# Optimization experiments

Hardware: AMD Instinct MI355X
Metric: run time of the kernel (lower is better)

## Reference

```python
import jax, jax.numpy as jnp
import numpy as np

EPS = 1e-3  # Q = eps * I(5) in the original module

def setup_inputs() -> dict:
    key = jax.random.key(0)
    k1, k2, k3 = jax.random.split(key, 3)
    B, n = 4194304, 5
    x = jax.random.normal(k1, (B, n), dtype=jnp.float32)
    # fc1 = nn.Linear(n, n): weight [n, n], bias [n]
    W = jax.random.normal(k2, (n, n), dtype=jnp.float32) * (1.0 / np.sqrt(n))
    b_fc = jax.random.normal(k3, (n,), dtype=jnp.float32) * 0.1
    return {"x": x, "W": W, "b_fc": b_fc}

def reference(x, W, b_fc):
    # h = fc1(x)  (the QP inequality RHS per sample)
    h = x @ W.T + b_fc  # [B, 5]
    # Per-sample QP: min_z 0.5*eps*||z||^2 + 1^T z  s.t.  -z <= h  (G = -I)
    # Separable closed form (exact solution cvxopt converges to):
    #   unconstrained minimizer z_i = -1/eps; constraint z_i >= -h_i
    #   => z_i = max(-h_i, -1/eps)
    z = jnp.maximum(-h, -1.0 / EPS)  # [B, 5] primal solutions
    return z
```

## Files before the change

kernel.cpp:

```cpp
#include <hip/hip_runtime.h>


#define BLOCK 256
#define WAVES_PER_BLOCK 4
#define F4_PER_WAVE 320

typedef float vf4 __attribute__((ext_vector_type(4)));

__global__ __launch_bounds__(BLOCK) void qpnet_kernel(
    const float* __restrict__ x,
    const float* __restrict__ W,
    const float* __restrict__ bfc,
    float* __restrict__ out,
    int total_f4)
{
    __shared__ __align__(16) float lds[BLOCK * 20];

    float w[5][5];
    float bias[5];
#pragma unroll
    for (int j = 0; j < 5; ++j) {
        bias[j] = bfc[j];
#pragma unroll
        for (int i = 0; i < 5; ++i) w[j][i] = W[j * 5 + i];
    }

    const int wave = threadIdx.x >> 6;
    const int lane = threadIdx.x & 63;
    float* __restrict__ wlds = &lds[wave * (64 * 20)];

    const int wave_id = blockIdx.x * WAVES_PER_BLOCK + wave;
    const int wbase = wave_id * F4_PER_WAVE;
    if (wbase >= total_f4) return;

    const vf4* __restrict__ xin  = reinterpret_cast<const vf4*>(x);
    vf4* __restrict__       zout = reinterpret_cast<vf4*>(out);

#pragma unroll
    for (int k = 0; k < 5; ++k) {
        *reinterpret_cast<vf4*>(&wlds[(k * 64 + lane) * 4]) = xin[wbase + k * 64 + lane];
    }
    asm volatile("s_waitcnt lgkmcnt(0)" ::: "memory");

    float v[20];
#pragma unroll
    for (int p = 0; p < 5; ++p) {
        *reinterpret_cast<vf4*>(&v[4 * p]) =
            *reinterpret_cast<const vf4*>(&wlds[lane * 20 + 4 * p]);
    }

#pragma unroll
    for (int k = 0; k < 4; ++k) {
        float t0 = bias[0], t1 = bias[1], t2 = bias[2], t3 = bias[3], t4 = bias[4];
#pragma unroll
        for (int i = 0; i < 5; ++i) {
            const float xv = v[k * 5 + i];
            t0 = fmaf(xv, w[0][i], t0);
            t1 = fmaf(xv, w[1][i], t1);
            t2 = fmaf(xv, w[2][i], t2);
            t3 = fmaf(xv, w[3][i], t3);
            t4 = fmaf(xv, w[4][i], t4);
        }
        v[k * 5 + 0] = fmaxf(-t0, -1000.0f);
        v[k * 5 + 1] = fmaxf(-t1, -1000.0f);
        v[k * 5 + 2] = fmaxf(-t2, -1000.0f);
        v[k * 5 + 3] = fmaxf(-t3, -1000.0f);
        v[k * 5 + 4] = fmaxf(-t4, -1000.0f);
    }

#pragma unroll
    for (int p = 0; p < 5; ++p) {
        *reinterpret_cast<vf4*>(&wlds[lane * 20 + 4 * p]) =
            *reinterpret_cast<const vf4*>(&v[4 * p]);
    }
    asm volatile("s_waitcnt lgkmcnt(0)" ::: "memory");

#pragma unroll
    for (int k = 0; k < 5; ++k) {
        zout[wbase + k * 64 + lane] =
            *reinterpret_cast<const vf4*>(&wlds[(k * 64 + lane) * 4]);
    }
}

extern "C" void kernel_launch(void* const* d_in, const int* in_sizes, int n_in,
                              void* d_out, int out_size, void* d_ws, size_t ws_size,
                              hipStream_t stream) {
    const float* x   = (const float*)d_in[0];
    const float* W   = (const float*)d_in[1];
    const float* bfc = (const float*)d_in[2];
    float* out = (float*)d_out;

    int total_f4 = in_sizes[0] / 4;
    int n_waves  = (total_f4 + F4_PER_WAVE - 1) / F4_PER_WAVE;
    int grid     = (n_waves + WAVES_PER_BLOCK - 1) / WAVES_PER_BLOCK;

    qpnet_kernel<<<grid, BLOCK, 0, stream>>>(x, W, bfc, out, total_f4);
}
```

Before: 152.0 us.

## Process four tiles per wave with register prefetch of next tile

Each wave now handles four consecutive 320-float4 tiles in a loop instead of one, and loads the next tile's input into registers while the current tile is transposed through LDS and computed. This spreads the per-wave setup (weight/bias loads) over more data and overlaps global loads with compute. It cuts the grid size by four, which may reduce the number of memory requests in flight across the device for this bandwidth-bound kernel.

Measured after the change: 155.6 us. 1.02x slower.

```diff
diff --git a/kernel.cpp b/kernel.cpp
--- a/kernel.cpp
+++ b/kernel.cpp
@@ -3,7 +3,8 @@
 
 #define BLOCK 256
 #define WAVES_PER_BLOCK 4
-#define F4_PER_WAVE 320
+#define F4_PER_TILE 320
+#define TILES_PER_WAVE 4
 
 typedef float vf4 __attribute__((ext_vector_type(4)));
 
@@ -30,55 +31,67 @@
     float* __restrict__ wlds = &lds[wave * (64 * 20)];
 
     const int wave_id = blockIdx.x * WAVES_PER_BLOCK + wave;
-    const int wbase = wave_id * F4_PER_WAVE;
-    if (wbase >= total_f4) return;
+    int tb = wave_id * (F4_PER_TILE * TILES_PER_WAVE);
+    if (tb >= total_f4) return;
 
     const vf4* __restrict__ xin  = reinterpret_cast<const vf4*>(x);
     vf4* __restrict__       zout = reinterpret_cast<vf4*>(out);
 
+    vf4 r[5];
 #pragma unroll
-    for (int k = 0; k < 5; ++k) {
-        *reinterpret_cast<vf4*>(&wlds[(k * 64 + lane) * 4]) = xin[wbase + k * 64 + lane];
-    }
-    asm volatile("s_waitcnt lgkmcnt(0)" ::: "memory");
+    for (int k = 0; k < 5; ++k) r[k] = xin[tb + k * 64 + lane];
 
-    float v[20];
-#pragma unroll
-    for (int p = 0; p < 5; ++p) {
-        *reinterpret_cast<vf4*>(&v[4 * p]) =
-            *reinterpret_cast<const vf4*>(&wlds[lane * 20 + 4 * p]);
-    }
+    for (int t = 0; t < TILES_PER_WAVE; ++t) {
+        const int cur = tb + t * F4_PER_TILE;
+        if (cur >= total_f4) break;
 
 #pragma unroll
-    for (int k = 0; k < 4; ++k) {
-        float t0 = bias[0], t1 = bias[1], t2 = bias[2], t3 = bias[3], t4 = bias[4];
+        for (int k = 0; k < 5; ++k)
+            *reinterpret_cast<vf4*>(&wlds[(k * 64 + lane) * 4]) = r[k];
+
+        const int nxt = cur + F4_PER_TILE;
+        if (t + 1 < TILES_PER_WAVE && nxt < total_f4) {
 #pragma unroll
-        for (int i = 0; i < 5; ++i) {
-            const float xv = v[k * 5 + i];
-            t0 = fmaf(xv, w[0][i], t0);
-            t1 = fmaf(xv, w[1][i], t1);
-            t2 = fmaf(xv, w[2][i], t2);
-            t3 = fmaf(xv, w[3][i], t3);
-            t4 = fmaf(xv, w[4][i], t4);
+            for (int k = 0; k < 5; ++k) r[k] = xin[nxt + k * 64 + lane];
         }
-        v[k * 5 + 0] = fmaxf(-t0, -1000.0f);
-        v[k * 5 + 1] = fmaxf(-t1, -1000.0f);
-        v[k * 5 + 2] = fmaxf(-t2, -1000.0f);
-        v[k * 5 + 3] = fmaxf(-t3, -1000.0f);
-        v[k * 5 + 4] = fmaxf(-t4, -1000.0f);
-    }
+
+        asm volatile("s_waitcnt lgkmcnt(0)" ::: "memory");
+
+        float v[20];
+#pragma unroll
+        for (int p = 0; p < 5; ++p)
+            *reinterpret_cast<vf4*>(&v[4 * p]) =
+                *reinterpret_cast<const vf4*>(&wlds[lane * 20 + 4 * p]);
 
 #pragma unroll
-    for (int p = 0; p < 5; ++p) {
-        *reinterpret_cast<vf4*>(&wlds[lane * 20 + 4 * p]) =
-            *reinterpret_cast<const vf4*>(&v[4 * p]);
-    }
-    asm volatile("s_waitcnt lgkmcnt(0)" ::: "memory");
+        for (int k = 0; k < 4; ++k) {
+            float t0 = bias[0], t1 = bias[1], t2 = bias[2], t3 = bias[3], t4 = bias[4];
+#pragma unroll
+            for (int i = 0; i < 5; ++i) {
+                const float xv = v[k * 5 + i];
+                t0 = fmaf(xv, w[0][i], t0);
+                t1 = fmaf(xv, w[1][i], t1);
+                t2 = fmaf(xv, w[2][i], t2);
+                t3 = fmaf(xv, w[3][i], t3);
+                t4 = fmaf(xv, w[4][i], t4);
+            }
+            v[k * 5 + 0] = fmaxf(-t0, -1000.0f);
+            v[k * 5 + 1] = fmaxf(-t1, -1000.0f);
+            v[k * 5 + 2] = fmaxf(-t2, -1000.0f);
+            v[k * 5 + 3] = fmaxf(-t3, -1000.0f);
+            v[k * 5 + 4] = fmaxf(-t4, -1000.0f);
+        }
 
 #pragma unroll
-    for (int k = 0; k < 5; ++k) {
-        zout[wbase + k * 64 + lane] =
-            *reinterpret_cast<const vf4*>(&wlds[(k * 64 + lane) * 4]);
+        for (int p = 0; p < 5; ++p)
+            *reinterpret_cast<vf4*>(&wlds[lane * 20 + 4 * p]) =
+                *reinterpret_cast<const vf4*>(&v[4 * p]);
+        asm volatile("s_waitcnt lgkmcnt(0)" ::: "memory");
+
+#pragma unroll
+        for (int k = 0; k < 5; ++k)
+            zout[cur + k * 64 + lane] =
+                *reinterpret_cast<const vf4*>(&wlds[(k * 64 + lane) * 4]);
     }
 }
 
@@ -91,7 +104,8 @@
     float* out = (float*)d_out;
 
     int total_f4 = in_sizes[0] / 4;
-    int n_waves  = (total_f4 + F4_PER_WAVE - 1) / F4_PER_WAVE;
+    int f4_per_wave = F4_PER_TILE * TILES_PER_WAVE;
+    int n_waves  = (total_f4 + f4_per_wave - 1) / f4_per_wave;
     int grid     = (n_waves + WAVES_PER_BLOCK - 1) / WAVES_PER_BLOCK;
 
     qpnet_kernel<<<grid, BLOCK, 0, stream>>>(x, W, bfc, out, total_f4);
```

## Replace LDS transpose with lane-shuffle stencil and grid-stride persistent waves

Applied to the files above, without the earlier changes.

Drops the shared-memory staging and transpose. Each lane now loads one float4 and takes its neighbours' float4s through shuffles, then applies a per-lane rotated 4x12 weight matrix to produce its four outputs. Work is split into 60-float4 segments so that rows never cross segment edges, and a grid-stride loop over a grid capped at 2048 blocks processes them. This removes the LDS traffic and the waits, but costs more FMAs per output, leaves 4 of 64 lanes idle, needs extra registers for the per-lane weights, and lowers per-wave memory parallelism.

Result: slower. 155.3 us (+2.2%).

```diff
diff --git a/kernel.cpp b/kernel.cpp
--- a/kernel.cpp
+++ b/kernel.cpp
@@ -2,8 +2,7 @@
 
 
 #define BLOCK 256
-#define WAVES_PER_BLOCK 4
-#define F4_PER_WAVE 320
+#define SEG_F4 60
 
 typedef float vf4 __attribute__((ext_vector_type(4)));
 
@@ -14,10 +13,7 @@
     float* __restrict__ out,
     int total_f4)
 {
-    __shared__ __align__(16) float lds[BLOCK * 20];
-
-    float w[5][5];
-    float bias[5];
+    float w[5][5], bias[5];
 #pragma unroll
     for (int j = 0; j < 5; ++j) {
         bias[j] = bfc[j];
@@ -25,60 +21,72 @@
         for (int i = 0; i < 5; ++i) w[j][i] = W[j * 5 + i];
     }
 
+    const int lane = threadIdx.x & 63;
     const int wave = threadIdx.x >> 6;
-    const int lane = threadIdx.x & 63;
-    float* __restrict__ wlds = &lds[wave * (64 * 20)];
 
-    const int wave_id = blockIdx.x * WAVES_PER_BLOCK + wave;
-    const int wbase = wave_id * F4_PER_WAVE;
-    if (wbase >= total_f4) return;
+    const int lq = lane % 5;
+    const int s  = (4 * lq) % 5;
+    float Wt[4][12], bq[4];
+#pragma unroll
+    for (int c = 0; c < 4; ++c) {
+        float bv = 0.0f;
+#pragma unroll
+        for (int k = 0; k < 12; ++k) Wt[c][k] = 0.0f;
+#pragma unroll
+        for (int sp = 0; sp < 5; ++sp) {
+            const int  jj  = (sp + c) % 5;
+            const int  st  = (sp + c < 5) ? (4 - sp) : (9 - sp);
+            const bool sel = (s == sp);
+            bv = sel ? bias[jj] : bv;
+#pragma unroll
+            for (int k = 0; k < 12; ++k) {
+                if (k >= st && k < st + 5) {
+                    const float cand = w[jj][k - st];
+                    Wt[c][k] = sel ? cand : Wt[c][k];
+                }
+            }
+        }
+        bq[c] = bv;
+    }
 
     const vf4* __restrict__ xin  = reinterpret_cast<const vf4*>(x);
     vf4* __restrict__       zout = reinterpret_cast<vf4*>(out);
 
+    const int gwave = blockIdx.x * (BLOCK / 64) + wave;
+    const int nwave = gridDim.x * (BLOCK / 64);
+    const int nseg  = (total_f4 + SEG_F4 - 1) / SEG_F4;
+    const int ll    = lane < 59 ? lane : 59;
+
+    for (int seg = gwave; seg < nseg; seg += nwave) {
+        const int s60 = seg * SEG_F4;
+
+        int li = s60 + ll;
+        if (li >= total_f4) li = total_f4 - 1;
+        const vf4 a = xin[li];
+
+        float vw[12];
 #pragma unroll
-    for (int k = 0; k < 5; ++k) {
-        *reinterpret_cast<vf4*>(&wlds[(k * 64 + lane) * 4]) = xin[wbase + k * 64 + lane];
-    }
-    asm volatile("s_waitcnt lgkmcnt(0)" ::: "memory");
+        for (int k = 0; k < 4; ++k) {
+            vw[4 + k] = a[k];
+            vw[k]     = __shfl_up(a[k], 1);
+            vw[8 + k] = __shfl_down(a[k], 1);
+        }
 
-    float v[20];
+        float zo[4];
 #pragma unroll
-    for (int p = 0; p < 5; ++p) {
-        *reinterpret_cast<vf4*>(&v[4 * p]) =
-            *reinterpret_cast<const vf4*>(&wlds[lane * 20 + 4 * p]);
-    }
+        for (int c = 0; c < 4; ++c) {
+            float acc = bq[c];
+#pragma unroll
+            for (int k = 0; k < 12; ++k) acc = fmaf(vw[k], Wt[c][k], acc);
+            zo[c] = fmaxf(-acc, -1000.0f);
+        }
 
-#pragma unroll
-    for (int k = 0; k < 4; ++k) {
-        float t0 = bias[0], t1 = bias[1], t2 = bias[2], t3 = bias[3], t4 = bias[4];
-#pragma unroll
-        for (int i = 0; i < 5; ++i) {
-            const float xv = v[k * 5 + i];
-            t0 = fmaf(xv, w[0][i], t0);
-            t1 = fmaf(xv, w[1][i], t1);
-            t2 = fmaf(xv, w[2][i], t2);
-            t3 = fmaf(xv, w[3][i], t3);
-            t4 = fmaf(xv, w[4][i], t4);
+        const int oi = s60 + lane;
+        if (lane < 60 && oi < total_f4) {
+            vf4 zv;
+            zv[0] = zo[0]; zv[1] = zo[1]; zv[2] = zo[2]; zv[3] = zo[3];
+            zout[oi] = zv;
         }
-        v[k * 5 + 0] = fmaxf(-t0, -1000.0f);
-        v[k * 5 + 1] = fmaxf(-t1, -1000.0f);
-        v[k * 5 + 2] = fmaxf(-t2, -1000.0f);
-        v[k * 5 + 3] = fmaxf(-t3, -1000.0f);
-        v[k * 5 + 4] = fmaxf(-t4, -1000.0f);
-    }
-
-#pragma unroll
-    for (int p = 0; p < 5; ++p) {
-        *reinterpret_cast<vf4*>(&wlds[lane * 20 + 4 * p]) =
-            *reinterpret_cast<const vf4*>(&v[4 * p]);
-    }
-    asm volatile("s_waitcnt lgkmcnt(0)" ::: "memory");
-
-#pragma unroll
-    for (int k = 0; k < 5; ++k) {
-        zout[wbase + k * 64 + lane] =
-            *reinterpret_cast<const vf4*>(&wlds[(k * 64 + lane) * 4]);
     }
 }
 
@@ -91,8 +99,9 @@
     float* out = (float*)d_out;
 
     int total_f4 = in_sizes[0] / 4;
-    int n_waves  = (total_f4 + F4_PER_WAVE - 1) / F4_PER_WAVE;
-    int grid     = (n_waves + WAVES_PER_BLOCK - 1) / WAVES_PER_BLOCK;
+    int nseg  = (total_f4 + SEG_F4 - 1) / SEG_F4;
+    int nblk  = (nseg + (BLOCK / 64) - 1) / (BLOCK / 64);
+    int grid  = nblk < 2048 ? nblk : 2048;
 
     qpnet_kernel<<<grid, BLOCK, 0, stream>>>(x, W, bfc, out, total_f4);
 }
```
